# Performance work log

Measured on AMD Instinct MI355X. Metric: run time of the kernel, lower is better.

## Reference

```python
import jax, jax.numpy as jnp
import numpy as np

B, S, D, H = 32, 512, 512, 1024  # batch, seq, latents_dims, hidden (=prod(out_dims))


def setup_inputs() -> dict:
    key = jax.random.key(0)
    ks = jax.random.split(key, 7)
    scale_ih = 1.0 / np.sqrt(D)
    scale_hh = 1.0 / np.sqrt(H)
    return {
        "x": jax.random.normal(ks[0], (B, S, D), dtype=jnp.float32),
        "h0": jax.random.uniform(ks[1], (B, H), dtype=jnp.float32),
        "c0": jax.random.uniform(ks[2], (B, H), dtype=jnp.float32),
        "W_ih": jax.random.normal(ks[3], (4 * H, D), dtype=jnp.float32) * scale_ih,
        "W_hh": jax.random.normal(ks[4], (4 * H, H), dtype=jnp.float32) * scale_hh,
        "b_ih": jax.random.normal(ks[5], (4 * H,), dtype=jnp.float32) * scale_hh,
        "b_hh": jax.random.normal(ks[6], (4 * H,), dtype=jnp.float32) * scale_hh,
    }


def reference(x, h0, c0, W_ih, W_hh, b_ih, b_hh):
    # Single-layer LSTM, PyTorch gate order (i, f, g, o).
    # Precompute the input projection for all timesteps in one GEMM: [B,S,4H]
    x_proj = jnp.einsum("bsd,gd->bsg", x, W_ih) + b_ih + b_hh
    xs = jnp.swapaxes(x_proj, 0, 1)  # [S, B, 4H]

    def step(carry, xp_t):
        h, c = carry  # [B, H] each
        gates = xp_t + h @ W_hh.T  # [B, 4H]
        i, f, g, o = jnp.split(gates, 4, axis=-1)
        i = jax.nn.sigmoid(i)
        f = jax.nn.sigmoid(f)
        g = jnp.tanh(g)
        o = jax.nn.sigmoid(o)
        c = f * c + i * g
        h = o * jnp.tanh(c)
        return (h, c), h

    _, hs = jax.lax.scan(step, (h0, c0), xs)  # hs: [S, B, H]
    out = jnp.swapaxes(hs, 0, 1)  # [B, S, H]
    # view(*x.shape[:2], *out_dims) with out_dims=[1024] is a no-op reshape
    return out.reshape(B, S, H)
```

## Files before the change

### kernel.cpp

```cpp
#include <hip/hip_runtime.h>

typedef __bf16 bf16_t;
typedef __bf16 bf16x8 __attribute__((ext_vector_type(8)));
typedef __bf16 bf16x4 __attribute__((ext_vector_type(4)));
typedef __bf16 bf16x2 __attribute__((ext_vector_type(2)));
typedef float f32x16 __attribute__((ext_vector_type(16)));
typedef int i32x4 __attribute__((ext_vector_type(4)));

#define SZ_XBF    (16384ull*512*2)
#define SZ_WIH    (4096ull*512*2)
#define SZ_WHH    (4096ull*1024*2)
#define SZ_XPROJ  (16384ull*4096*2)
#define SZ_HTR    (513ull*32*1024*2)
#define OFF_XBF   (0ull)
#define OFF_WIH   (OFF_XBF + SZ_XBF)
#define OFF_WHH   (OFF_WIH + SZ_WIH)
#define OFF_XPROJ (OFF_WHH + SZ_WHH)
#define OFF_HTR   (OFF_XPROJ + SZ_XPROJ)


__global__ __launch_bounds__(256) void convert_pack(
    const float* __restrict__ x, const float* __restrict__ h0,
    const float* __restrict__ Wih, const float* __restrict__ Whh,
    bf16_t* __restrict__ xbf, bf16_t* __restrict__ wihbf,
    bf16_t* __restrict__ whhbf, bf16_t* __restrict__ htr)
{
  long long v = (long long)blockIdx.x * 256 + threadIdx.x;
  if (v < 2097152LL) {
    long long fi = v * 4;
    int b = (int)(fi >> 18);
    int rem = (int)(fi & 0x3FFFF);
    int s = rem >> 9, d = rem & 511;
    float4 f = *(const float4*)(x + fi);
    bf16x4 o; o.x = (bf16_t)f.x; o.y = (bf16_t)f.y; o.z = (bf16_t)f.z; o.w = (bf16_t)f.w;
    *(bf16x4*)(xbf + ((long long)(s*32 + b)*512 + d)) = o;
  } else if (v < 2621440LL) {
    long long fi = (v - 2097152LL) * 4;
    float4 f = *(const float4*)(Wih + fi);
    bf16x4 o; o.x = (bf16_t)f.x; o.y = (bf16_t)f.y; o.z = (bf16_t)f.z; o.w = (bf16_t)f.w;
    *(bf16x4*)(wihbf + fi) = o;
  } else if (v < 3670016LL) {
    long long fi = (v - 2621440LL) * 4;
    float4 f = *(const float4*)(Whh + fi);
    bf16x4 o; o.x = (bf16_t)f.x; o.y = (bf16_t)f.y; o.z = (bf16_t)f.z; o.w = (bf16_t)f.w;
    *(bf16x4*)(whhbf + fi) = o;
  } else if (v < 3678208LL) {
    long long fi = (v - 3670016LL) * 4;
    int b = (int)(fi >> 10), c = (int)(fi & 1023);
    float4 f = *(const float4*)(h0 + fi);
    bf16x4 o; o.x = (bf16_t)f.x; o.y = (bf16_t)f.y; o.z = (bf16_t)f.z; o.w = (bf16_t)f.w;
    *(bf16x4*)(htr + (long long)(c >> 4) * 512 + b * 16 + (c & 15)) = o;
  } else if (v < 5775360LL) {
    long long idx = v - 3678208LL;
    *(int4*)(htr + 32768LL + idx * 8) = make_int4(-1, -1, -1, -1);
  }
}

__global__ __launch_bounds__(256) void xproj_gemm(
    const bf16_t* __restrict__ Xb, const bf16_t* __restrict__ Wb,
    const float* __restrict__ bih, const float* __restrict__ bhh,
    bf16_t* __restrict__ XP)
{
  __shared__ bf16_t As[128*64];
  __shared__ bf16_t Bs[128*64];
  const int tid = threadIdx.x;
  const int lane = tid & 63, wave = tid >> 6;
  const int mhalf = wave & 1, nhalf = wave >> 1;
  const int l31 = lane & 31, khi = lane >> 5;
  const int m0 = blockIdx.x * 128, n0 = blockIdx.y * 128;

  f32x16 acc[2][2] = {};

  for (int kb = 0; kb < 8; ++kb) {
    const int k0 = kb * 64;
    __syncthreads();
#pragma unroll
    for (int j = 0; j < 4; ++j) {
      int cid = j * 256 + tid;
      int r = cid >> 3, bs = cid & 7;
      int bb = bs ^ (r & 7);
      *(bf16x8*)(As + cid * 8) = *(const bf16x8*)(Xb + (long long)(m0 + r) * 512 + k0 + bb * 8);
      *(bf16x8*)(Bs + cid * 8) = *(const bf16x8*)(Wb + (long long)(n0 + r) * 512 + k0 + bb * 8);
    }
    __syncthreads();
#pragma unroll
    for (int ks = 0; ks < 4; ++ks) {
      int blk = ks * 2 + khi;
      bf16x8 af[2], bfr[2];
#pragma unroll
      for (int mt = 0; mt < 2; ++mt) {
        int r = mhalf * 64 + mt * 32 + l31;
        af[mt] = *(const bf16x8*)(As + (r * 8 + (blk ^ (r & 7))) * 8);
      }
#pragma unroll
      for (int nt = 0; nt < 2; ++nt) {
        int r = nhalf * 64 + nt * 32 + l31;
        bfr[nt] = *(const bf16x8*)(Bs + (r * 8 + (blk ^ (r & 7))) * 8);
      }
#pragma unroll
      for (int mt = 0; mt < 2; ++mt)
#pragma unroll
        for (int nt = 0; nt < 2; ++nt)
          acc[mt][nt] = __builtin_amdgcn_mfma_f32_32x32x16_bf16(af[mt], bfr[nt], acc[mt][nt], 0, 0, 0);
    }
  }
#pragma unroll
  for (int nt = 0; nt < 2; ++nt) {
    int ng = n0 + nhalf * 64 + nt * 32 + l31;
    float bias = bih[ng] + bhh[ng];
#pragma unroll
    for (int mt = 0; mt < 2; ++mt) {
#pragma unroll
      for (int r = 0; r < 16; ++r) {
        int row = (r & 3) + 8 * (r >> 2) + 4 * khi;
        long long mg = m0 + mhalf * 64 + mt * 32 + row;
        XP[mg * 4096 + ng] = (bf16_t)(acc[mt][nt][r] + bias);
      }
    }
  }
}

__device__ __forceinline__ float sigf(float x) { return 1.0f / (1.0f + __expf(-x)); }
__device__ __forceinline__ float tanhfast(float x) {
  float e = __expf(-2.0f * fabsf(x));
  float t = (1.0f - e) / (1.0f + e);
  return copysignf(t, x);
}
__device__ __forceinline__ unsigned umax2(unsigned a, unsigned b) { return a > b ? a : b; }
__device__ __forceinline__ unsigned umax4(i32x4 v) {
  return umax2(umax2((unsigned)v[0], (unsigned)v[1]),
               umax2((unsigned)v[2], (unsigned)v[3]));
}

#define LD16(dst, ptr, OFF) \
  asm volatile("global_load_dwordx4 %0, %1, off offset:" OFF " sc0 sc1" \
               : "=v"(dst) : "v"(ptr) : "memory")

__global__ __launch_bounds__(256, 1) void lstm_rec(
    const bf16_t* __restrict__ Whh_b, const bf16_t* __restrict__ XP,
    const float* __restrict__ c0, float* __restrict__ OUT,
    bf16_t* __restrict__ HTR)
{
  const int tid = threadIdx.x;
  const int lane = tid & 63, wave = tid >> 6;
  const int kq = wave;
  const int wg = blockIdx.x;
  const int l31 = lane & 31, khi = lane >> 5;

  const int g0row = (l31 >> 4) * 1024 + wg * 16 + (l31 & 15);
  const int g1row = (2 + (l31 >> 4)) * 1024 + wg * 16 + (l31 & 15);
  const int kqb = kq * 256 + khi * 8;
  bf16x8 w0[16], w1[16];
#pragma unroll
  for (int s = 0; s < 16; ++s) {
    w0[s] = *(const bf16x8*)(Whh_b + (long long)g0row * 1024 + kqb + s * 16);
    w1[s] = *(const bf16x8*)(Whh_b + (long long)g1row * 1024 + kqb + s * 16);
  }

  const char* abase = (const char*)HTR + kq * 16384 + l31 * 32 + khi * 16;
  const char* pbase = (const char*)HTR + kq * 16384 + (lane & 15) * 1024 + 1020;

  __shared__ float gLb[2][4][32][65];
  const int m_e = tid >> 3;
  const int jp = (tid & 7) * 2;
  float cr0 = c0[m_e * 1024 + wg * 16 + jp];
  float cr1 = c0[m_e * 1024 + wg * 16 + jp + 1];

  float xp[4][2];
  {
    const bf16_t* xpb = XP + (long long)m_e * 4096 + wg * 16 + jp;
#pragma unroll
    for (int g = 0; g < 4; ++g) {
      bf16x2 v = *(const bf16x2*)(xpb + g * 1024);
      xp[g][0] = (float)v.x; xp[g][1] = (float)v.y;
    }
  }

  float po0 = 0.0f, po1 = 0.0f;

  for (int t = 0; t < 512; ++t) {
    {
      const char* pbt = pbase + ((long long)t << 16);
      unsigned pv;
      for (;;) {
        asm volatile("global_load_dword %0, %1, off sc0 sc1"
                     : "=v"(pv) : "v"(pbt) : "memory");
        asm volatile("s_waitcnt vmcnt(0)" ::: "memory");
        if (__all((int)(pv != 0xFFFFFFFFu))) break;
      }
    }

    const char* p0 = abase + ((long long)t << 16);
    const char* p1 = p0 + 4096;
    const char* p2 = p0 + 8192;
    const char* p3 = p0 + 12288;
    i32x4 a[16];
    for (;;) {
      LD16(a[0],  p0, "0"); LD16(a[1],  p0, "1024"); LD16(a[2],  p0, "2048"); LD16(a[3],  p0, "3072");
      LD16(a[4],  p1, "0"); LD16(a[5],  p1, "1024"); LD16(a[6],  p1, "2048"); LD16(a[7],  p1, "3072");
      LD16(a[8],  p2, "0"); LD16(a[9],  p2, "1024"); LD16(a[10], p2, "2048"); LD16(a[11], p2, "3072");
      LD16(a[12], p3, "0"); LD16(a[13], p3, "1024"); LD16(a[14], p3, "2048"); LD16(a[15], p3, "3072");
      asm volatile("s_waitcnt vmcnt(0)" ::: "memory");
      __builtin_amdgcn_sched_barrier(0);
      unsigned mA = 0, mB = 0, mC = 0, mD = 0;
#pragma unroll
      for (int s = 0; s < 16; s += 4) {
        mA = umax2(mA, umax4(a[s]));
        mB = umax2(mB, umax4(a[s + 1]));
        mC = umax2(mC, umax4(a[s + 2]));
        mD = umax2(mD, umax4(a[s + 3]));
      }
      unsigned mx = umax2(umax2(mA, mB), umax2(mC, mD));
      if (!__any((int)(mx == 0xFFFFFFFFu))) break;
    }

    if (t > 0)
      *(float2*)(OUT + ((long long)m_e * 512 + (t - 1)) * 1024 + wg * 16 + jp) =
          make_float2(po0, po1);

    f32x16 acc0 = {}, acc1 = {};
#pragma unroll
    for (int s = 0; s < 16; ++s) {
      bf16x8 af = __builtin_bit_cast(bf16x8, a[s]);
      acc0 = __builtin_amdgcn_mfma_f32_32x32x16_bf16(af, w0[s], acc0, 0, 0, 0);
      acc1 = __builtin_amdgcn_mfma_f32_32x32x16_bf16(af, w1[s], acc1, 0, 0, 0);
    }

    float (*gp)[65] = gLb[t & 1][kq];
#pragma unroll
    for (int r = 0; r < 16; ++r) {
      int mm = (r & 3) + 8 * (r >> 2) + 4 * khi;
      gp[mm][l31]      = acc0[r];
      gp[mm][32 + l31] = acc1[r];
    }
    __syncthreads();

    float (*ge)[32][65] = gLb[t & 1];
    float hv[2];
    {
      float ir  = ge[0][m_e][jp]      + ge[1][m_e][jp]      + ge[2][m_e][jp]      + ge[3][m_e][jp]      + xp[0][0];
      float fr  = ge[0][m_e][16 + jp] + ge[1][m_e][16 + jp] + ge[2][m_e][16 + jp] + ge[3][m_e][16 + jp] + xp[1][0];
      float gr  = ge[0][m_e][32 + jp] + ge[1][m_e][32 + jp] + ge[2][m_e][32 + jp] + ge[3][m_e][32 + jp] + xp[2][0];
      float orr = ge[0][m_e][48 + jp] + ge[1][m_e][48 + jp] + ge[2][m_e][48 + jp] + ge[3][m_e][48 + jp] + xp[3][0];
      float c = sigf(fr) * cr0 + sigf(ir) * tanhfast(gr);
      cr0 = c;
      hv[0] = sigf(orr) * tanhfast(c);
    }
    {
      int j = jp + 1;
      float ir  = ge[0][m_e][j]      + ge[1][m_e][j]      + ge[2][m_e][j]      + ge[3][m_e][j]      + xp[0][1];
      float fr  = ge[0][m_e][16 + j] + ge[1][m_e][16 + j] + ge[2][m_e][16 + j] + ge[3][m_e][16 + j] + xp[1][1];
      float gr  = ge[0][m_e][32 + j] + ge[1][m_e][32 + j] + ge[2][m_e][32 + j] + ge[3][m_e][32 + j] + xp[2][1];
      float orr = ge[0][m_e][48 + j] + ge[1][m_e][48 + j] + ge[2][m_e][48 + j] + ge[3][m_e][48 + j] + xp[3][1];
      float c = sigf(fr) * cr1 + sigf(ir) * tanhfast(gr);
      cr1 = c;
      hv[1] = sigf(orr) * tanhfast(c);
    }

    {
      bf16x2 h2; h2.x = (bf16_t)hv[0]; h2.y = (bf16_t)hv[1];
      unsigned int u = __builtin_bit_cast(unsigned int, h2);
      unsigned int* dst = (unsigned int*)(HTR + (long long)(t + 1) * 32768 +
                                          (long long)wg * 512 + m_e * 16 + jp);
      __hip_atomic_store(dst, u, __ATOMIC_RELAXED, __HIP_MEMORY_SCOPE_AGENT);
    }
    po0 = hv[0]; po1 = hv[1];

    if (t < 511) {
      const bf16_t* xpb = XP + ((long long)(t + 1) * 32 + m_e) * 4096 + wg * 16 + jp;
#pragma unroll
      for (int g = 0; g < 4; ++g) {
        bf16x2 v = *(const bf16x2*)(xpb + g * 1024);
        xp[g][0] = (float)v.x; xp[g][1] = (float)v.y;
      }
    }
  }
  *(float2*)(OUT + ((long long)m_e * 512 + 511) * 1024 + wg * 16 + jp) =
      make_float2(po0, po1);
}

extern "C" void kernel_launch(void* const* d_in, const int* in_sizes, int n_in,
                              void* d_out, int out_size, void* d_ws, size_t ws_size,
                              hipStream_t stream)
{
  const float* x   = (const float*)d_in[0];
  const float* h0  = (const float*)d_in[1];
  const float* c0  = (const float*)d_in[2];
  const float* Wih = (const float*)d_in[3];
  const float* Whh = (const float*)d_in[4];
  const float* bih = (const float*)d_in[5];
  const float* bhh = (const float*)d_in[6];
  float* out = (float*)d_out;

  char* ws = (char*)d_ws;
  bf16_t* xbf   = (bf16_t*)(ws + OFF_XBF);
  bf16_t* wihbf = (bf16_t*)(ws + OFF_WIH);
  bf16_t* whhbf = (bf16_t*)(ws + OFF_WHH);
  bf16_t* xproj = (bf16_t*)(ws + OFF_XPROJ);
  bf16_t* htr   = (bf16_t*)(ws + OFF_HTR);

  convert_pack<<<22560, 256, 0, stream>>>(x, h0, Wih, Whh, xbf, wihbf, whhbf, htr);
  xproj_gemm<<<dim3(128, 32), 256, 0, stream>>>(xbf, wihbf, bih, bhh, xproj);
  lstm_rec<<<64, 256, 0, stream>>>(whhbf, xproj, c0, out, htr);
}
```

Before: 1.691 ms.

## Replace sentinel polling with per-workgroup ready flags in LSTM recurrence

```diff
diff --git a/kernel.cpp b/kernel.cpp
--- a/kernel.cpp
+++ b/kernel.cpp
@@ -12,18 +12,21 @@
 #define SZ_WHH    (4096ull*1024*2)
 #define SZ_XPROJ  (16384ull*4096*2)
 #define SZ_HTR    (513ull*32*1024*2)
+#define SZ_RDY    (33024ull*4)
 #define OFF_XBF   (0ull)
 #define OFF_WIH   (OFF_XBF + SZ_XBF)
 #define OFF_WHH   (OFF_WIH + SZ_WIH)
 #define OFF_XPROJ (OFF_WHH + SZ_WHH)
 #define OFF_HTR   (OFF_XPROJ + SZ_XPROJ)
+#define OFF_RDY   (OFF_HTR + SZ_HTR)
 
 
 __global__ __launch_bounds__(256) void convert_pack(
     const float* __restrict__ x, const float* __restrict__ h0,
     const float* __restrict__ Wih, const float* __restrict__ Whh,
     bf16_t* __restrict__ xbf, bf16_t* __restrict__ wihbf,
-    bf16_t* __restrict__ whhbf, bf16_t* __restrict__ htr)
+    bf16_t* __restrict__ whhbf, bf16_t* __restrict__ htr,
+    int* __restrict__ rdy)
 {
   long long v = (long long)blockIdx.x * 256 + threadIdx.x;
   if (v < 2097152LL) {
@@ -53,6 +56,9 @@
   } else if (v < 5775360LL) {
     long long idx = v - 3678208LL;
     *(int4*)(htr + 32768LL + idx * 8) = make_int4(-1, -1, -1, -1);
+  } else if (v < 5783616LL) {
+    long long idx = v - 5775360LL;
+    *(int4*)(rdy + idx * 4) = make_int4(0, 0, 0, 0);
   }
 }
 
@@ -139,7 +145,7 @@
 __global__ __launch_bounds__(256, 1) void lstm_rec(
     const bf16_t* __restrict__ Whh_b, const bf16_t* __restrict__ XP,
     const float* __restrict__ c0, float* __restrict__ OUT,
-    bf16_t* __restrict__ HTR)
+    bf16_t* __restrict__ HTR, int* RDY)
 {
   const int tid = threadIdx.x;
   const int lane = tid & 63, wave = tid >> 6;
@@ -158,7 +164,7 @@
   }
 
   const char* abase = (const char*)HTR + kq * 16384 + l31 * 32 + khi * 16;
-  const char* pbase = (const char*)HTR + kq * 16384 + (lane & 15) * 1024 + 1020;
+  const char* rbase = (const char*)RDY + lane * 4;
 
   __shared__ float gLb[2][4][32][65];
   const int m_e = tid >> 3;
@@ -179,29 +185,24 @@
   float po0 = 0.0f, po1 = 0.0f;
 
   for (int t = 0; t < 512; ++t) {
-    {
-      const char* pbt = pbase + ((long long)t << 16);
-      unsigned pv;
+    if (t) {
+      const char* rp = rbase + ((long long)t << 8);
+      unsigned rv;
       for (;;) {
         asm volatile("global_load_dword %0, %1, off sc0 sc1"
-                     : "=v"(pv) : "v"(pbt) : "memory");
+                     : "=v"(rv) : "v"(rp) : "memory");
         asm volatile("s_waitcnt vmcnt(0)" ::: "memory");
-        if (__all((int)(pv != 0xFFFFFFFFu))) break;
-      }
-    }
-
-    const char* p0 = abase + ((long long)t << 16);
-    const char* p1 = p0 + 4096;
-    const char* p2 = p0 + 8192;
-    const char* p3 = p0 + 12288;
+        if (__all((int)(rv != 0u))) break;
+      }
+    }
+
+    const char* pb = abase + ((long long)t << 16);
     i32x4 a[16];
-    for (;;) {
-      LD16(a[0],  p0, "0"); LD16(a[1],  p0, "1024"); LD16(a[2],  p0, "2048"); LD16(a[3],  p0, "3072");
-      LD16(a[4],  p1, "0"); LD16(a[5],  p1, "1024"); LD16(a[6],  p1, "2048"); LD16(a[7],  p1, "3072");
-      LD16(a[8],  p2, "0"); LD16(a[9],  p2, "1024"); LD16(a[10], p2, "2048"); LD16(a[11], p2, "3072");
-      LD16(a[12], p3, "0"); LD16(a[13], p3, "1024"); LD16(a[14], p3, "2048"); LD16(a[15], p3, "3072");
-      asm volatile("s_waitcnt vmcnt(0)" ::: "memory");
-      __builtin_amdgcn_sched_barrier(0);
+#pragma unroll
+    for (int s = 0; s < 16; ++s)
+      a[s] = *(const i32x4*)(pb + s * 1024);
+
+    {
       unsigned mA = 0, mB = 0, mC = 0, mD = 0;
 #pragma unroll
       for (int s = 0; s < 16; s += 4) {
@@ -211,7 +212,30 @@
         mD = umax2(mD, umax4(a[s + 3]));
       }
       unsigned mx = umax2(umax2(mA, mB), umax2(mC, mD));
-      if (!__any((int)(mx == 0xFFFFFFFFu))) break;
+      if (__any((int)(mx == 0xFFFFFFFFu))) {
+        const char* p0 = pb;
+        const char* p1 = pb + 4096;
+        const char* p2 = pb + 8192;
+        const char* p3 = pb + 12288;
+        for (;;) {
+          LD16(a[0],  p0, "0"); LD16(a[1],  p0, "1024"); LD16(a[2],  p0, "2048"); LD16(a[3],  p0, "3072");
+          LD16(a[4],  p1, "0"); LD16(a[5],  p1, "1024"); LD16(a[6],  p1, "2048"); LD16(a[7],  p1, "3072");
+          LD16(a[8],  p2, "0"); LD16(a[9],  p2, "1024"); LD16(a[10], p2, "2048"); LD16(a[11], p2, "3072");
+          LD16(a[12], p3, "0"); LD16(a[13], p3, "1024"); LD16(a[14], p3, "2048"); LD16(a[15], p3, "3072");
+          asm volatile("s_waitcnt vmcnt(0)" ::: "memory");
+          __builtin_amdgcn_sched_barrier(0);
+          unsigned nA = 0, nB = 0, nC = 0, nD = 0;
+#pragma unroll
+          for (int s = 0; s < 16; s += 4) {
+            nA = umax2(nA, umax4(a[s]));
+            nB = umax2(nB, umax4(a[s + 1]));
+            nC = umax2(nC, umax4(a[s + 2]));
+            nD = umax2(nD, umax4(a[s + 3]));
+          }
+          unsigned nx = umax2(umax2(nA, nB), umax2(nC, nD));
+          if (!__any((int)(nx == 0xFFFFFFFFu))) break;
+        }
+      }
     }
 
     if (t > 0)
@@ -274,6 +298,11 @@
         xp[g][0] = (float)v.x; xp[g][1] = (float)v.y;
       }
     }
+
+    __syncthreads();
+    if (tid == 0 && t < 511)
+      __hip_atomic_store(&RDY[(t + 1) * 64 + wg], 1, __ATOMIC_RELAXED,
+                         __HIP_MEMORY_SCOPE_AGENT);
   }
   *(float2*)(OUT + ((long long)m_e * 512 + 511) * 1024 + wg * 16 + jp) =
       make_float2(po0, po1);
@@ -298,8 +327,9 @@
   bf16_t* whhbf = (bf16_t*)(ws + OFF_WHH);
   bf16_t* xproj = (bf16_t*)(ws + OFF_XPROJ);
   bf16_t* htr   = (bf16_t*)(ws + OFF_HTR);
-
-  convert_pack<<<22560, 256, 0, stream>>>(x, h0, Wih, Whh, xbf, wihbf, whhbf, htr);
+  int* rdy      = (int*)(ws + OFF_RDY);
+
+  convert_pack<<<22593, 256, 0, stream>>>(x, h0, Wih, Whh, xbf, wihbf, whhbf, htr, rdy);
   xproj_gemm<<<dim3(128, 32), 256, 0, stream>>>(xbf, wihbf, bih, bhh, xproj);
-  lstm_rec<<<64, 256, 0, stream>>>(whhbf, xproj, c0, out, htr);
-}
+  lstm_rec<<<64, 256, 0, stream>>>(whhbf, xproj, c0, out, htr, rdy);
+}
```

New measurement: 2.761 ms. 63.3% more time.
